# Kernel optimization log

Measured on AMD Instinct MI355X. Metric: run time of the kernel, lower is better.

## Reference

```python
import jax, jax.numpy as jnp
import numpy as np

B, N, D_IN, D_OUT = 32, 256, 512, 2048
RANK, K, H_CTRL = 12, 16, 192
RESIDUAL_SCALE = 1.0


def setup_inputs() -> dict:
    key = jax.random.key(0)
    ks = jax.random.split(key, 12)
    x = jax.random.normal(ks[0], (B, N, D_IN), dtype=jnp.float32)
    shared_weight = 0.02 * jax.random.normal(ks[1], (D_OUT, D_IN), dtype=jnp.float32)
    bias = jnp.zeros((D_OUT,), dtype=jnp.float32)
    # orthogonal init for U_0 [out, in] via QR of a Gaussian
    g = jax.random.normal(ks[2], (D_OUT, D_IN), dtype=jnp.float32)
    U0, _ = jnp.linalg.qr(g, mode='reduced')  # columns orthonormal, out>=in
    left_basis = 0.02 * jax.random.normal(ks[3], (K, D_OUT, RANK), dtype=jnp.float32)
    right_basis = 0.02 * jax.random.normal(ks[4], (K, D_IN, RANK), dtype=jnp.float32)
    ctrl_dim = 3 * D_IN  # cls_mean_var pooling
    W1 = (1.0 / np.sqrt(ctrl_dim)) * jax.random.normal(ks[5], (ctrl_dim, H_CTRL), dtype=jnp.float32)
    b1 = jnp.zeros((H_CTRL,), dtype=jnp.float32)
    Wc = (1.0 / np.sqrt(H_CTRL)) * jax.random.normal(ks[6], (H_CTRL, K), dtype=jnp.float32)
    bc = jnp.zeros((K,), dtype=jnp.float32)
    Wg = (1.0 / np.sqrt(H_CTRL)) * jax.random.normal(ks[7], (H_CTRL, 1), dtype=jnp.float32)
    bg = jnp.zeros((1,), dtype=jnp.float32)
    return {"x": x, "shared_weight": shared_weight, "bias": bias, "U0": U0,
            "left_basis": left_basis, "right_basis": right_basis,
            "W1": W1, "b1": b1, "Wc": Wc, "bc": bc, "Wg": Wg, "bg": bg}


def _controller(z, W1, b1, Wc, bc, Wg, bg):
    # MLP controller: coeff head (linear) + gate head (sigmoid)
    h = jax.nn.gelu(z @ W1 + b1)
    coeff = h @ Wc + bc            # [B, K]
    gate = jax.nn.sigmoid(h @ Wg + bg)  # [B, 1]
    return coeff, gate


def reference(x, shared_weight, bias, U0, left_basis, right_basis, W1, b1, Wc, bc, Wg, bg):
    # conditioning signal: cls + mean + var (unbiased=False)
    cls = x[:, 0]
    mean = x.mean(axis=1)
    var = x.var(axis=1)  # population variance, matches unbiased=False
    z = jnp.concatenate([cls, mean, var], axis=-1)  # [B, 3*D_IN]
    coeff, gate = _controller(z, W1, b1, Wc, bc, Wg, bg)

    # tangent dictionary
    raw = jnp.einsum('kmr,kdr->kmd', left_basis, right_basis)        # [K, M, D]
    ut_raw = jnp.einsum('mi,kmj->kij', U0, raw)                       # U0^T @ raw: [K, D, D]
    sym = 0.5 * (ut_raw + jnp.swapaxes(ut_raw, -2, -1))
    tangent = raw - jnp.einsum('mi,kij->kmj', U0, sym)                # [K, M, D]
    norm = jnp.sqrt(jnp.sum(tangent * tangent, axis=(1, 2), keepdims=True))
    tangent = tangent / jnp.maximum(norm, 1e-6)

    # per-sample candidate + QR retraction (Stiefel)
    delta = jnp.einsum('bk,kmd->bmd', coeff, tangent)                 # [B, M, D]
    candidate = U0[None] + RESIDUAL_SCALE * delta
    q, r = jnp.linalg.qr(candidate, mode='reduced')                   # q: [B, M, D]
    sign = jnp.sign(jnp.diagonal(r, axis1=-2, axis2=-1))              # [B, D]
    sign = jnp.where(sign == 0, jnp.ones_like(sign), sign)
    dynamic_weight = q * sign[..., None, :]
    residual_weight = dynamic_weight - U0[None]                       # [B, M, D]

    out = x @ shared_weight.T + bias                                  # [B, N, M]
    residual_out = jnp.einsum('bnd,bmd->bnm', x, residual_weight)     # [B, N, M]
    return out + gate.reshape(-1, 1, 1) * residual_out
```

## Files before the change

### kernel.cpp

```cpp
#include <hip/hip_runtime.h>
#include <math.h>

#define B_    32
#define N_    256
#define DIN   512
#define DOUT  2048
#define RANK_ 12
#define K_    16
#define HC    192
#define CD    1536
#define P1    192
#define P2    384

typedef short short8 __attribute__((ext_vector_type(8)));
typedef float f32x4 __attribute__((ext_vector_type(4)));

__device__ inline short bf16r(float f) {
  unsigned u = __float_as_uint(f);
  unsigned r = (u + 0x7FFFu + ((u >> 16) & 1u)) >> 16;
  return (short)r;
}
__device__ inline float b16f(short s) {
  unsigned u = ((unsigned)(unsigned short)s) << 16;
  return __uint_as_float(u);
}

__global__ void k_stats(const float* __restrict__ x, float* __restrict__ z) {
  int b = blockIdx.x, d = threadIdx.x;
  const float* xb = x + (size_t)b * N_ * DIN;
  float s = 0.f, s2 = 0.f;
  for (int n = 0; n < N_; ++n) {
    float t = xb[(size_t)n * DIN + d];
    s += t; s2 += t * t;
  }
  float mean = s * (1.0f / N_);
  float var = s2 * (1.0f / N_) - mean * mean;
  float* zb = z + (size_t)b * CD;
  zb[d] = xb[d];
  zb[DIN + d] = mean;
  zb[2 * DIN + d] = var;
}

__global__ void k_controller(const float* __restrict__ z, const float* __restrict__ W1,
                             const float* __restrict__ b1, const float* __restrict__ Wc,
                             const float* __restrict__ bc, const float* __restrict__ Wg,
                             const float* __restrict__ bg, float* __restrict__ coeff,
                             float* __restrict__ gate) {
  int b = blockIdx.x, j = threadIdx.x;
  __shared__ float zs[CD];
  __shared__ float hs[HC];
  const float* zb = z + (size_t)b * CD;
  for (int i = j; i < CD; i += HC) zs[i] = zb[i];
  __syncthreads();
  float acc = b1[j];
  for (int d = 0; d < CD; ++d) acc = fmaf(zs[d], W1[(size_t)d * HC + j], acc);
  float x3 = acc * acc * acc;
  float hj = 0.5f * acc * (1.0f + tanhf(0.7978845608028654f * (acc + 0.044715f * x3)));
  hs[j] = hj;
  __syncthreads();
  if (j < K_) {
    float c = bc[j];
    for (int t = 0; t < HC; ++t) c = fmaf(hs[t], Wc[t * K_ + j], c);
    coeff[b * K_ + j] = c;
  } else if (j == K_) {
    float g = bg[0];
    for (int t = 0; t < HC; ++t) g = fmaf(hs[t], Wg[t], g);
    gate[b] = 1.0f / (1.0f + expf(-g));
  }
}

__global__ void k_copy_bases(const float* __restrict__ leftb, const float* __restrict__ rightb,
                             float* __restrict__ Lcat, float* __restrict__ E) {
  int idx = blockIdx.x * 256 + threadIdx.x;
  const int totL = DOUT * P1;
  const int totR = DIN * P1;
  if (idx < totL) {
    int m = idx / P1, j = idx - m * P1;
    int k = j / RANK_, r = j - k * RANK_;
    Lcat[idx] = leftb[((size_t)k * DOUT + m) * RANK_ + r];
  } else if (idx < totL + totR) {
    int i2 = idx - totL;
    int d = i2 / P1, j = i2 - d * P1;
    int k = j / RANK_, r = j - k * RANK_;
    E[(size_t)d * P2 + j] = rightb[((size_t)k * DIN + d) * RANK_ + r];
  }
}

__global__ void k_pack_B(const float* __restrict__ Wsh, const float* __restrict__ U0,
                         const float* __restrict__ LcatF, short* __restrict__ Bcat) {
  int idx = blockIdx.x * 256 + threadIdx.x;
  if (idx >= DOUT * 152) return;
  int row = idx / 152, g = idx - row * 152;
  const float* src;
  if (g < 64)       src = Wsh + (size_t)row * DIN + g * 8;
  else if (g < 128) src = U0 + (size_t)row * DIN + (g - 64) * 8;
  else              src = LcatF + (size_t)row * P1 + (g - 128) * 8;
  short8 o;
#pragma unroll
  for (int e = 0; e < 8; ++e) o[e] = bf16r(src[e]);
  *(short8*)(Bcat + (size_t)row * 1216 + g * 8) = o;
}

__global__ __launch_bounds__(256) void k_gemm_tn(const float* __restrict__ A,
                                                 const float* __restrict__ B,
                                                 float* __restrict__ C,
                                                 int M, int N, int Kd, int lda, int ldb, int ldc) {
  __shared__ float As[32][33], Bs[32][33];
  int i0 = blockIdx.x * 32, j0 = blockIdx.y * 32;
  int t = threadIdx.x;
  int ii = t & 31, j4 = (t >> 5) * 4;
  float acc[4] = {0.f, 0.f, 0.f, 0.f};
  for (int kb = 0; kb < Kd; kb += 32) {
    for (int idx = t; idx < 1024; idx += 256) {
      int kk = idx >> 5, c = idx & 31;
      As[kk][c] = A[(size_t)(kb + kk) * lda + i0 + c];
      Bs[kk][c] = B[(size_t)(kb + kk) * ldb + j0 + c];
    }
    __syncthreads();
#pragma unroll 8
    for (int kk = 0; kk < 32; ++kk) {
      float a = As[kk][ii];
#pragma unroll
      for (int q = 0; q < 4; ++q) acc[q] = fmaf(a, Bs[kk][j4 + q], acc[q]);
    }
    __syncthreads();
  }
#pragma unroll
  for (int q = 0; q < 4; ++q) C[(size_t)(i0 + ii) * ldc + j0 + j4 + q] = acc[q];
}

__global__ void k_norms(const float* __restrict__ GLL, const float* __restrict__ GE,
                        float* __restrict__ norms) {
  int k = blockIdx.x, t = threadIdx.x;
  float s1 = 0.f, s2 = 0.f, s3 = 0.f;
  for (int idx = t; idx < RANK_ * RANK_; idx += 64) {
    int r = idx / RANK_, s = idx - r * RANK_;
    int p = k * RANK_ + r, q = k * RANK_ + s;
    float gll = GLL[p * P1 + q];
    float grr = GE[p * P2 + q];
    float gpp = GE[(P1 + p) * P2 + (P1 + q)];
    float gpr = GE[(P1 + p) * P2 + q];
    float gprt = GE[(P1 + q) * P2 + p];
    s1 += gll * grr;
    s2 += gpp * grr;
    s3 += gpr * gprt;
  }
#pragma unroll
  for (int off = 32; off > 0; off >>= 1) {
    s1 += __shfl_down(s1, off);
    s2 += __shfl_down(s2, off);
    s3 += __shfl_down(s3, off);
  }
  if (t == 0) norms[k] = sqrtf(fmaxf(s1 - 0.5f * (s2 + s3), 0.0f));
}

__global__ void k_cprime(const float* __restrict__ coeff, const float* __restrict__ norms,
                         float* __restrict__ cp) {
  int t = threadIdx.x;
  if (t < B_ * K_) {
    int k = t & 15;
    cp[t] = coeff[t] / fmaxf(norms[k], 1e-6f);
  }
}

__global__ void k_m0b(const float* __restrict__ GLL, const float* __restrict__ GE,
                      short* __restrict__ M0b) {
  int idx = blockIdx.x * 256 + threadIdx.x;
  if (idx >= P2 * P2) return;
  int p = idx / P2, q = idx - p * P2;
  float v;
  if (p < P1) {
    if (q < P1) v = GLL[p * P1 + q] - 0.75f * GE[(P1 + p) * P2 + (P1 + q)];
    else        v = -0.25f * GE[(P1 + p) * P2 + (q - P1)];
  } else {
    if (q < P1) v = -0.25f * GE[(P1 + q) * P2 + (p - P1)];
    else        v = 0.25f * GE[(p - P1) * P2 + (q - P1)];
  }
  M0b[idx] = bf16r(v);
}

__global__ void k_packE(const float* __restrict__ E, short* __restrict__ Eb16,
                        short* __restrict__ Etb16) {
  int idx = blockIdx.x * 256 + threadIdx.x;
  if (idx >= DIN * P2) return;
  int d = idx / P2, q = idx - d * P2;
  short v = bf16r(E[idx]);
  Eb16[idx] = v;
  Etb16[(size_t)q * DIN + d] = v;
}

__global__ void k_packEc(const float* __restrict__ E, const float* __restrict__ cp,
                         short* __restrict__ Ecb) {
  int idx = blockIdx.x * 256 + threadIdx.x;
  if (idx >= B_ * DIN * 48) return;
  int b = idx / (DIN * 48);
  int rem = idx - b * DIN * 48;
  int d = rem / 48, g = rem - d * 48;
  int q0 = g * 8;
  const float* src = E + (size_t)d * P2 + q0;
  const float* cpb = cp + b * K_;
  short8 o;
#pragma unroll
  for (int e = 0; e < 8; ++e) {
    int q = q0 + e;
    int kidx = (q % P1) / RANK_;
    o[e] = bf16r(src[e] * cpb[kidx]);
  }
  *(short8*)(Ecb + ((size_t)b * DIN + d) * P2 + q0) = o;
}

template<int MSZ, int NSZ, int KD>
__global__ __launch_bounds__(256) void k_mf_nt16(const short* __restrict__ A,
                                                 const short* __restrict__ B,
                                                 short* __restrict__ C) {
  int b = blockIdx.z;
  const short* Ab = A + (size_t)b * MSZ * KD;
  short* Cb = C + (size_t)b * MSZ * NSZ;
  int c0 = blockIdx.x * 64, r0 = blockIdx.y * 64;
  __shared__ short As[64][40], Bs[64][40];
  int t = threadIdx.x;
  int l = t & 63, wid = t >> 6;
  int wr = wid >> 1, wc = wid & 1;
  int fr = l & 15, fq = l >> 4;
  int row = t >> 2, cg = t & 3;
  f32x4 acc[2][2] = {};
  for (int kt = 0; kt < KD / 32; ++kt) {
    *(short8*)&As[row][cg * 8] = *(const short8*)(Ab + (size_t)(r0 + row) * KD + kt * 32 + cg * 8);
    *(short8*)&Bs[row][cg * 8] = *(const short8*)(B + (size_t)(c0 + row) * KD + kt * 32 + cg * 8);
    __syncthreads();
    short8 af[2], bf[2];
#pragma unroll
    for (int m = 0; m < 2; ++m) af[m] = *(const short8*)&As[wr * 32 + m * 16 + fr][fq * 8];
#pragma unroll
    for (int n = 0; n < 2; ++n) bf[n] = *(const short8*)&Bs[wc * 32 + n * 16 + fr][fq * 8];
#pragma unroll
    for (int m = 0; m < 2; ++m)
#pragma unroll
      for (int n = 0; n < 2; ++n)
        acc[m][n] = __builtin_amdgcn_mfma_f32_16x16x32_bf16(af[m], bf[n], acc[m][n], 0, 0, 0);
    __syncthreads();
  }
#pragma unroll
  for (int m = 0; m < 2; ++m)
#pragma unroll
    for (int n = 0; n < 2; ++n)
#pragma unroll
      for (int j = 0; j < 4; ++j)
        Cb[(size_t)(r0 + wr * 32 + m * 16 + fq * 4 + j) * NSZ + c0 + wc * 32 + n * 16 + fr] =
            bf16r(acc[m][n][j]);
}

__global__ __launch_bounds__(256) void k_mf_G(const short* __restrict__ H,
                                              const short* __restrict__ Ec,
                                              float* __restrict__ G) {
  int b = blockIdx.z;
  const short* Ab = H + (size_t)b * DIN * P2;
  const short* Bb = Ec + (size_t)b * DIN * P2;
  float* Gb = G + (size_t)b * DIN * DIN;
  int c0 = blockIdx.x * 64, r0 = blockIdx.y * 64;
  __shared__ short As[64][40], Bs[64][40];
  int t = threadIdx.x;
  int l = t & 63, wid = t >> 6;
  int wr = wid >> 1, wc = wid & 1;
  int fr = l & 15, fq = l >> 4;
  int row = t >> 2, cg = t & 3;
  f32x4 acc[2][2] = {};
  for (int kt = 0; kt < P2 / 32; ++kt) {
    *(short8*)&As[row][cg * 8] = *(const short8*)(Ab + (size_t)(r0 + row) * P2 + kt * 32 + cg * 8);
    *(short8*)&Bs[row][cg * 8] = *(const short8*)(Bb + (size_t)(c0 + row) * P2 + kt * 32 + cg * 8);
    __syncthreads();
    short8 af[2], bf[2];
#pragma unroll
    for (int m = 0; m < 2; ++m) af[m] = *(const short8*)&As[wr * 32 + m * 16 + fr][fq * 8];
#pragma unroll
    for (int n = 0; n < 2; ++n) bf[n] = *(const short8*)&Bs[wc * 32 + n * 16 + fr][fq * 8];
#pragma unroll
    for (int m = 0; m < 2; ++m)
#pragma unroll
      for (int n = 0; n < 2; ++n)
        acc[m][n] = __builtin_amdgcn_mfma_f32_16x16x32_bf16(af[m], bf[n], acc[m][n], 0, 0, 0);
    __syncthreads();
  }
#pragma unroll
  for (int m = 0; m < 2; ++m)
#pragma unroll
    for (int n = 0; n < 2; ++n)
#pragma unroll
      for (int j = 0; j < 4; ++j) {
        int gr = r0 + wr * 32 + m * 16 + fq * 4 + j;
        int gc = c0 + wc * 32 + n * 16 + fr;
        Gb[(size_t)gr * DIN + gc] = acc[m][n][j] + (gr == gc ? 1.0f : 0.0f);
      }
}

__global__ __launch_bounds__(64) void k_chol_dp2(float* __restrict__ G, float* __restrict__ Wd,
                                                 int j0) {
  int b = blockIdx.y;
  int role = blockIdx.x;
  float* Gb = G + (size_t)b * DIN * DIN;
  __shared__ float D[64][65];
  __shared__ float Wls[64][65];
  __shared__ float dinvs[64];
  int t = threadIdx.x;
#pragma unroll 8
  for (int i = 0; i < 64; ++i) D[i][t] = Gb[(size_t)(j0 + i) * DIN + j0 + t];
  __syncthreads();
  {
    float col[64];
#pragma unroll
    for (int i = 0; i < 64; ++i) col[i] = D[i][t];
#pragma unroll
    for (int j = 0; j < 64; ++j) {
      float djj = __shfl(col[j], j);
      float rjj = sqrtf(fmaxf(djj, 1e-30f));
      float rinv = 1.0f / rjj;
      if (t == j) col[j] = rjj;
      else if (t > j) col[j] *= rinv;
      float djt = col[j];
#pragma unroll
      for (int i = j + 1; i < 64; ++i) {
        float rji = __shfl(col[j], i);
        if (i <= t) col[i] = fmaf(-rji, djt, col[i]);
      }
    }
#pragma unroll
    for (int i = 0; i < 64; ++i) D[i][t] = (i <= t) ? col[i] : 0.0f;
    dinvs[t] = 1.0f / col[t];
  }
  __syncthreads();
  if (role == 0) {
#pragma unroll 4
    for (int i = 0; i < 64; ++i) Wls[i][t] = 0.0f;
    Wls[t][t] = dinvs[t];
    for (int i = 62; i >= 0; --i) {
      float s = 0.0f;
      for (int j = i + 1; j < 64; ++j) s = fmaf(D[i][j], Wls[j][t], s);
      if (t > i) Wls[i][t] = -s * dinvs[i];
    }
    float* Wp = Wd + ((size_t)b * 8 + (j0 >> 6)) * 4096;
#pragma unroll 4
    for (int i = 0; i < 64; ++i) Wp[i * 64 + t] = Wls[i][t];
  } else {
    int c = j0 + 64 + (role - 1) * 64 + t;
    float a[64];
#pragma unroll
    for (int i = 0; i < 64; ++i) a[i] = Gb[(size_t)(j0 + i) * DIN + c];
#pragma unroll
    for (int j = 0; j < 64; ++j) {
      float aj = a[j] * dinvs[j];
      a[j] = aj;
#pragma unroll
      for (int i = j + 1; i < 64; ++i) a[i] = fmaf(-D[j][i], aj, a[i]);
    }
#pragma unroll
    for (int i = 0; i < 64; ++i) Gb[(size_t)(j0 + i) * DIN + c] = a[i];
  }
}

__global__ __launch_bounds__(256) void k_chol_tr(float* __restrict__ G, int j0, int nt) {
  int b = blockIdx.y;
  int pi = blockIdx.x;
  int ti = 0, accum = 0;
  while (pi >= accum + (nt - ti)) { accum += nt - ti; ++ti; }
  int tc = ti + (pi - accum);
  float* Gb = G + (size_t)b * DIN * DIN;
  __shared__ float As[64][65], Bs[64][65];
  int t = threadIdx.x;
  int ibase = j0 + 64 + ti * 64, cbase = j0 + 64 + tc * 64;
  for (int idx = t; idx < 4096; idx += 256) {
    int j = idx >> 6, c = idx & 63;
    As[j][c] = Gb[(size_t)(j0 + j) * DIN + ibase + c];
    Bs[j][c] = Gb[(size_t)(j0 + j) * DIN + cbase + c];
  }
  __syncthreads();
  int tx = t & 15, ty = t >> 4;
  float acc[4][4] = {};
#pragma unroll 8
  for (int k = 0; k < 64; ++k) {
    float a[4], bv[4];
#pragma unroll
    for (int u = 0; u < 4; ++u) a[u] = As[k][ty * 4 + u];
#pragma unroll
    for (int v = 0; v < 4; ++v) bv[v] = Bs[k][tx * 4 + v];
#pragma unroll
    for (int u = 0; u < 4; ++u)
#pragma unroll
      for (int v = 0; v < 4; ++v) acc[u][v] = fmaf(a[u], bv[v], acc[u][v]);
  }
#pragma unroll
  for (int u = 0; u < 4; ++u) {
    size_t ro = (size_t)(ibase + ty * 4 + u) * DIN + cbase + tx * 4;
#pragma unroll
    for (int v = 0; v < 4; ++v) Gb[ro + v] -= acc[u][v];
  }
}

__global__ __launch_bounds__(256) void k_trif(const float* __restrict__ x, const float* __restrict__ G,
                                              const float* __restrict__ Wd, short* __restrict__ ybf,
                                              short* __restrict__ ycb) {
  int b = blockIdx.y;
  int n0 = blockIdx.x * 16;
  const float* R = G + (size_t)b * DIN * DIN;
  const float* xb = x + ((size_t)b * N_ + n0) * DIN;
  __shared__ float Yl[16][517];
  __shared__ float Rs[16][65];
  __shared__ float Wds[64][65];
  __shared__ float Ytmp[16][69];
  int t = threadIdx.x;
  for (int idx = t; idx < 16 * DIN; idx += 256)
    Yl[idx >> 9][idx & 511] = xb[(size_t)(idx >> 9) * DIN + (idx & 511)];
  __syncthreads();
  int r = t & 15, cg = t >> 4;
  for (int p = 7; p >= 0; --p) {
    int j0 = p * 64;
    int kN = DIN - j0 - 64;
    float acc[4] = {0.f, 0.f, 0.f, 0.f};
    for (int kb = 0; kb < kN; kb += 16) {
      for (int idx = t; idx < 1024; idx += 256) {
        int kk = idx & 15, c = idx >> 4;
        Rs[kk][c] = R[(size_t)(j0 + c) * DIN + j0 + 64 + kb + kk];
      }
      __syncthreads();
#pragma unroll
      for (int kk = 0; kk < 16; ++kk) {
        float a = Yl[r][j0 + 64 + kb + kk];
#pragma unroll
        for (int v = 0; v < 4; ++v) acc[v] = fmaf(a, Rs[kk][cg * 4 + v], acc[v]);
      }
      __syncthreads();
    }
#pragma unroll
    for (int v = 0; v < 4; ++v) Ytmp[r][cg * 4 + v] = Yl[r][j0 + cg * 4 + v] - acc[v];
    const float* Wp = Wd + ((size_t)b * 8 + p) * 4096;
    for (int idx = t; idx < 4096; idx += 256) Wds[idx >> 6][idx & 63] = Wp[idx];
    __syncthreads();
    float o[4] = {0.f, 0.f, 0.f, 0.f};
#pragma unroll 8
    for (int jj = 0; jj < 64; ++jj) {
      float a = Ytmp[r][jj];
#pragma unroll
      for (int v = 0; v < 4; ++v) o[v] = fmaf(a, Wds[cg * 4 + v][jj], o[v]);
    }
    __syncthreads();
#pragma unroll
    for (int v = 0; v < 4; ++v) Yl[r][j0 + cg * 4 + v] = o[v];
    __syncthreads();
  }
  for (int idx = t; idx < 16 * DIN; idx += 256) {
    int rr = idx >> 9, c = idx & 511;
    float yv = Yl[rr][c];
    float xv = xb[(size_t)rr * DIN + c];
    size_t gi = ((size_t)b * N_ + n0 + rr) * DIN + c;
    ybf[gi] = bf16r(yv);
    ycb[gi] = bf16r(yv - xv);
  }
}

__global__ void k_uv2(const float* __restrict__ cp, const float* __restrict__ gate,
                      const short* __restrict__ yE16, short* __restrict__ vb) {
  int idx = blockIdx.x * 256 + threadIdx.x;
  if (idx >= B_ * N_ * P1) return;
  int q = idx % P1;
  int bn = idx / P1;
  int b = bn >> 8;
  float yR = b16f(yE16[(size_t)bn * P2 + q]);
  vb[idx] = bf16r(gate[b] * cp[b * K_ + q / RANK_] * yR);
}

__global__ __launch_bounds__(256) void k_mf_w(const short* __restrict__ yE16,
                                              const short* __restrict__ Eb,
                                              const short* __restrict__ ycb,
                                              const float* __restrict__ cp,
                                              const float* __restrict__ gate,
                                              short* __restrict__ wb) {
  int b = blockIdx.z;
  const short* yEb = yE16 + (size_t)b * N_ * P2;
  int c0 = blockIdx.x * 64, r0 = blockIdx.y * 64;
  __shared__ short As[64][40], Bs[64][40];
  __shared__ float cps[K_];
  int t = threadIdx.x;
  if (t < K_) cps[t] = 0.5f * cp[b * K_ + t];
  int l = t & 63, wid = t >> 6;
  int wr = wid >> 1, wc = wid & 1;
  int fr = l & 15, fq = l >> 4;
  int row = t >> 2, cg = t & 3;
  f32x4 acc[2][2] = {};
  __syncthreads();
  for (int kt = 0; kt < P2 / 32; ++kt) {
    int ksrc0 = (kt * 32 + P1) % P2;
    short8 raw = *(const short8*)(yEb + (size_t)(r0 + row) * P2 + ksrc0 + cg * 8);
    short8 oa;
#pragma unroll
    for (int e = 0; e < 8; ++e) {
      int q = kt * 32 + cg * 8 + e;
      int kidx = (q % P1) / RANK_;
      oa[e] = bf16r(b16f(raw[e]) * cps[kidx]);
    }
    *(short8*)&As[row][cg * 8] = oa;
    *(short8*)&Bs[row][cg * 8] = *(const short8*)(Eb + (size_t)(c0 + row) * P2 + kt * 32 + cg * 8);
    __syncthreads();
    short8 af[2], bf[2];
#pragma unroll
    for (int m = 0; m < 2; ++m) af[m] = *(const short8*)&As[wr * 32 + m * 16 + fr][fq * 8];
#pragma unroll
    for (int n = 0; n < 2; ++n) bf[n] = *(const short8*)&Bs[wc * 32 + n * 16 + fr][fq * 8];
#pragma unroll
    for (int m = 0; m < 2; ++m)
#pragma unroll
      for (int n = 0; n < 2; ++n)
        acc[m][n] = __builtin_amdgcn_mfma_f32_16x16x32_bf16(af[m], bf[n], acc[m][n], 0, 0, 0);
    __syncthreads();
  }
  float gt = gate[b];
#pragma unroll
  for (int m = 0; m < 2; ++m)
#pragma unroll
    for (int n = 0; n < 2; ++n)
#pragma unroll
      for (int j = 0; j < 4; ++j) {
        int gr = r0 + wr * 32 + m * 16 + fq * 4 + j;
        int gc = c0 + wc * 32 + n * 16 + fr;
        size_t gi = ((size_t)b * N_ + gr) * DIN + gc;
        wb[gi] = bf16r(gt * (b16f(ycb[gi]) - acc[m][n][j]));
      }
}

__device__ inline short8 loadA8(const float* __restrict__ x, const short* __restrict__ wb,
                                const short* __restrict__ vb, int grow, int k0) {
  if (k0 < 512) {
    const float* p = x + (size_t)grow * 512 + k0;
    float4 f0 = *(const float4*)p;
    float4 f1 = *(const float4*)(p + 4);
    short8 o;
    o[0] = bf16r(f0.x); o[1] = bf16r(f0.y); o[2] = bf16r(f0.z); o[3] = bf16r(f0.w);
    o[4] = bf16r(f1.x); o[5] = bf16r(f1.y); o[6] = bf16r(f1.z); o[7] = bf16r(f1.w);
    return o;
  } else if (k0 < 1024) {
    return *(const short8*)(wb + (size_t)grow * 512 + k0 - 512);
  } else {
    return *(const short8*)(vb + (size_t)grow * 192 + k0 - 1024);
  }
}

__global__ __launch_bounds__(256) void k_final(
    const float* __restrict__ x, const short* __restrict__ wb, const short* __restrict__ vb,
    const short* __restrict__ Bcat, const float* __restrict__ bias, float* __restrict__ out) {
  __shared__ short As[2][4096];
  __shared__ short Bs[2][4096];
  int t = threadIdx.x;
  int c0 = blockIdx.x * 128;
  int r0 = blockIdx.y * 128;
  int l = t & 63, wid = t >> 6;
  int wr = wid >> 1, wc = wid & 1;
  int fr = l & 15, fq = l >> 4;
  f32x4 acc[4][4] = {};
  short8 ra0, ra1, rb0, rb1;
  const int row0 = t >> 2, c8 = t & 3;
  const int row1 = row0 + 64;
  ra0 = loadA8(x, wb, vb, r0 + row0, c8 * 8);
  ra1 = loadA8(x, wb, vb, r0 + row1, c8 * 8);
  rb0 = *(const short8*)(Bcat + (size_t)(c0 + row0) * 1216 + c8 * 8);
  rb1 = *(const short8*)(Bcat + (size_t)(c0 + row1) * 1216 + c8 * 8);
  *(short8*)&As[0][row0 * 32 + c8 * 8] = ra0;
  *(short8*)&As[0][row1 * 32 + c8 * 8] = ra1;
  *(short8*)&Bs[0][row0 * 32 + c8 * 8] = rb0;
  *(short8*)&Bs[0][row1 * 32 + c8 * 8] = rb1;
  __syncthreads();
  for (int kt = 0; kt < 38; ++kt) {
    int cur = kt & 1;
    if (kt + 1 < 38) {
      int k0 = (kt + 1) * 32;
      ra0 = loadA8(x, wb, vb, r0 + row0, k0 + c8 * 8);
      ra1 = loadA8(x, wb, vb, r0 + row1, k0 + c8 * 8);
      rb0 = *(const short8*)(Bcat + (size_t)(c0 + row0) * 1216 + k0 + c8 * 8);
      rb1 = *(const short8*)(Bcat + (size_t)(c0 + row1) * 1216 + k0 + c8 * 8);
    }
    short8 af[4], bf[4];
#pragma unroll
    for (int m = 0; m < 4; ++m)
      af[m] = *(const short8*)&As[cur][(wr * 64 + m * 16 + fr) * 32 + fq * 8];
#pragma unroll
    for (int n = 0; n < 4; ++n)
      bf[n] = *(const short8*)&Bs[cur][(wc * 64 + n * 16 + fr) * 32 + fq * 8];
#pragma unroll
    for (int m = 0; m < 4; ++m)
#pragma unroll
      for (int n = 0; n < 4; ++n)
        acc[m][n] = __builtin_amdgcn_mfma_f32_16x16x32_bf16(af[m], bf[n], acc[m][n], 0, 0, 0);
    __syncthreads();
    if (kt + 1 < 38) {
      int nxt = cur ^ 1;
      *(short8*)&As[nxt][row0 * 32 + c8 * 8] = ra0;
      *(short8*)&As[nxt][row1 * 32 + c8 * 8] = ra1;
      *(short8*)&Bs[nxt][row0 * 32 + c8 * 8] = rb0;
      *(short8*)&Bs[nxt][row1 * 32 + c8 * 8] = rb1;
    }
    __syncthreads();
  }
#pragma unroll
  for (int n = 0; n < 4; ++n) {
    int col = c0 + wc * 64 + n * 16 + fr;
    float bv = bias[col];
#pragma unroll
    for (int m = 0; m < 4; ++m) {
      int rbase = r0 + wr * 64 + m * 16 + fq * 4;
#pragma unroll
      for (int j = 0; j < 4; ++j)
        out[(size_t)(rbase + j) * DOUT + col] = acc[m][n][j] + bv;
    }
  }
}

extern "C" void kernel_launch(void* const* d_in, const int* in_sizes, int n_in,
                              void* d_out, int out_size, void* d_ws, size_t ws_size,
                              hipStream_t stream) {
  (void)in_sizes; (void)n_in; (void)out_size; (void)ws_size;
  const float* x     = (const float*)d_in[0];
  const float* Wsh   = (const float*)d_in[1];
  const float* bias  = (const float*)d_in[2];
  const float* U0    = (const float*)d_in[3];
  const float* leftb = (const float*)d_in[4];
  const float* rightb= (const float*)d_in[5];
  const float* W1    = (const float*)d_in[6];
  const float* b1    = (const float*)d_in[7];
  const float* Wc    = (const float*)d_in[8];
  const float* bc    = (const float*)d_in[9];
  const float* Wg    = (const float*)d_in[10];
  const float* bg    = (const float*)d_in[11];
  float* out = (float*)d_out;

  float* wsf = (float*)d_ws;
  float* z     = wsf + 0;
  float* coeff = wsf + 49152;
  float* gate  = wsf + 49664;
  float* norms = wsf + 49728;
  float* cp    = wsf + 49792;
  float* LcatF = wsf + 50304;
  float* E     = wsf + 443520;
  float* GLL   = wsf + 640128;
  float* GE    = wsf + 676992;
  short* M0b16 = (short*)(wsf + 824448);
  short* Eb16  = (short*)(wsf + 898176);
  short* Etb16 = (short*)(wsf + 996480);
  short* wb    = (short*)(wsf + 1094784);
  short* Ecb   = (short*)(wsf + 3191936);
  short* ybf   = (short*)(wsf + 3191936);
  short* vb    = (short*)(wsf + 5289088);
  short* Hb16  = (short*)(wsf + 6337664);
  short* ycb   = (short*)(wsf + 6337664);
  short* Bcat  = (short*)(wsf + 9483392);
  float* G = out;
  float* Wd = out + 8388608;
  short* yE16 = (short*)(out + 8388608 + 1048576);

  k_stats<<<B_, DIN, 0, stream>>>(x, z);
  k_controller<<<B_, HC, 0, stream>>>(z, W1, b1, Wc, bc, Wg, bg, coeff, gate);
  k_copy_bases<<<(DOUT * P1 + DIN * P1 + 255) / 256, 256, 0, stream>>>(leftb, rightb, LcatF, E);
  k_pack_B<<<(DOUT * 152 + 255) / 256, 256, 0, stream>>>(Wsh, U0, LcatF, Bcat);
  k_gemm_tn<<<dim3(DIN / 32, P1 / 32), 256, 0, stream>>>(U0, LcatF, E + P1, DIN, P1, DOUT, DIN, P1, P2);
  k_gemm_tn<<<dim3(P1 / 32, P1 / 32), 256, 0, stream>>>(LcatF, LcatF, GLL, P1, P1, DOUT, P1, P1, P1);
  k_gemm_tn<<<dim3(P2 / 32, P2 / 32), 256, 0, stream>>>(E, E, GE, P2, P2, DIN, P2, P2, P2);
  k_norms<<<K_, 64, 0, stream>>>(GLL, GE, norms);
  k_cprime<<<1, 512, 0, stream>>>(coeff, norms, cp);
  k_m0b<<<(P2 * P2 + 255) / 256, 256, 0, stream>>>(GLL, GE, M0b16);
  k_packE<<<(DIN * P2 + 255) / 256, 256, 0, stream>>>(E, Eb16, Etb16);
  k_packEc<<<(B_ * DIN * 48 + 255) / 256, 256, 0, stream>>>(E, cp, Ecb);
  k_mf_nt16<DIN, P2, P2><<<dim3(P2 / 64, DIN / 64, B_), 256, 0, stream>>>(Ecb, M0b16, Hb16);
  k_mf_G<<<dim3(DIN / 64, DIN / 64, B_), 256, 0, stream>>>(Hb16, Ecb, G);
  for (int p = 0; p < 8; ++p) {
    int j0 = p * 64;
    int nt = 7 - p;
    k_chol_dp2<<<dim3(nt + 1, B_), 64, 0, stream>>>(G, Wd, j0);
    if (nt > 0)
      k_chol_tr<<<dim3(nt * (nt + 1) / 2, B_), 256, 0, stream>>>(G, j0, nt);
  }
  k_trif<<<dim3(N_ / 16, B_), 256, 0, stream>>>(x, G, Wd, ybf, ycb);
  k_mf_nt16<N_, P2, DIN><<<dim3(P2 / 64, N_ / 64, B_), 256, 0, stream>>>(ybf, Etb16, yE16);
  k_uv2<<<(B_ * N_ * P1 + 255) / 256, 256, 0, stream>>>(cp, gate, yE16, vb);
  k_mf_w<<<dim3(DIN / 64, N_ / 64, B_), 256, 0, stream>>>(yE16, Eb16, ycb, cp, gate, wb);
  k_final<<<dim3(DOUT / 128, (B_ * N_) / 128), 256, 0, stream>>>(x, wb, vb, Bcat, bias, out);
}
```

Baseline: 1.745 ms.

## Merge preprocessing kernels into fewer launches and fuse yE GEMM with uv epilogue

Folds the twelve small preprocessing launches (stats, controller, base copies, packing, small GEMMs, norms, cprime, M0/Ec packing) into five multi-role kernels that dispatch work by block index. Independent stages now share a launch. It also fuses the yE bf16 GEMM with the gate/coefficient scaling that produces vb, which removes one pass over yE. Separately, the triangular-solve kernel now stages 64-wide R tiles instead of 16-wide ones, so it synchronises less often but uses more shared memory per block.

```diff
diff --git a/kernel.cpp b/kernel.cpp
--- a/kernel.cpp
+++ b/kernel.cpp
@@ -25,89 +25,50 @@
   return __uint_as_float(u);
 }
 
-__global__ void k_stats(const float* __restrict__ x, float* __restrict__ z) {
-  int b = blockIdx.x, d = threadIdx.x;
-  const float* xb = x + (size_t)b * N_ * DIN;
-  float s = 0.f, s2 = 0.f;
-  for (int n = 0; n < N_; ++n) {
-    float t = xb[(size_t)n * DIN + d];
-    s += t; s2 += t * t;
-  }
-  float mean = s * (1.0f / N_);
-  float var = s2 * (1.0f / N_) - mean * mean;
-  float* zb = z + (size_t)b * CD;
-  zb[d] = xb[d];
-  zb[DIN + d] = mean;
-  zb[2 * DIN + d] = var;
-}
-
-__global__ void k_controller(const float* __restrict__ z, const float* __restrict__ W1,
-                             const float* __restrict__ b1, const float* __restrict__ Wc,
-                             const float* __restrict__ bc, const float* __restrict__ Wg,
-                             const float* __restrict__ bg, float* __restrict__ coeff,
-                             float* __restrict__ gate) {
-  int b = blockIdx.x, j = threadIdx.x;
-  __shared__ float zs[CD];
-  __shared__ float hs[HC];
-  const float* zb = z + (size_t)b * CD;
-  for (int i = j; i < CD; i += HC) zs[i] = zb[i];
-  __syncthreads();
-  float acc = b1[j];
-  for (int d = 0; d < CD; ++d) acc = fmaf(zs[d], W1[(size_t)d * HC + j], acc);
-  float x3 = acc * acc * acc;
-  float hj = 0.5f * acc * (1.0f + tanhf(0.7978845608028654f * (acc + 0.044715f * x3)));
-  hs[j] = hj;
-  __syncthreads();
-  if (j < K_) {
-    float c = bc[j];
-    for (int t = 0; t < HC; ++t) c = fmaf(hs[t], Wc[t * K_ + j], c);
-    coeff[b * K_ + j] = c;
-  } else if (j == K_) {
-    float g = bg[0];
-    for (int t = 0; t < HC; ++t) g = fmaf(hs[t], Wg[t], g);
-    gate[b] = 1.0f / (1.0f + expf(-g));
-  }
-}
-
-__global__ void k_copy_bases(const float* __restrict__ leftb, const float* __restrict__ rightb,
-                             float* __restrict__ Lcat, float* __restrict__ E) {
-  int idx = blockIdx.x * 256 + threadIdx.x;
-  const int totL = DOUT * P1;
-  const int totR = DIN * P1;
-  if (idx < totL) {
-    int m = idx / P1, j = idx - m * P1;
-    int k = j / RANK_, r = j - k * RANK_;
-    Lcat[idx] = leftb[((size_t)k * DOUT + m) * RANK_ + r];
-  } else if (idx < totL + totR) {
-    int i2 = idx - totL;
-    int d = i2 / P1, j = i2 - d * P1;
-    int k = j / RANK_, r = j - k * RANK_;
-    E[(size_t)d * P2 + j] = rightb[((size_t)k * DIN + d) * RANK_ + r];
-  }
-}
-
-__global__ void k_pack_B(const float* __restrict__ Wsh, const float* __restrict__ U0,
-                         const float* __restrict__ LcatF, short* __restrict__ Bcat) {
-  int idx = blockIdx.x * 256 + threadIdx.x;
-  if (idx >= DOUT * 152) return;
-  int row = idx / 152, g = idx - row * 152;
-  const float* src;
-  if (g < 64)       src = Wsh + (size_t)row * DIN + g * 8;
-  else if (g < 128) src = U0 + (size_t)row * DIN + (g - 64) * 8;
-  else              src = LcatF + (size_t)row * P1 + (g - 128) * 8;
-  short8 o;
-#pragma unroll
-  for (int e = 0; e < 8; ++e) o[e] = bf16r(src[e]);
-  *(short8*)(Bcat + (size_t)row * 1216 + g * 8) = o;
-}
-
-__global__ __launch_bounds__(256) void k_gemm_tn(const float* __restrict__ A,
-                                                 const float* __restrict__ B,
-                                                 float* __restrict__ C,
-                                                 int M, int N, int Kd, int lda, int ldb, int ldc) {
-  __shared__ float As[32][33], Bs[32][33];
-  int i0 = blockIdx.x * 32, j0 = blockIdx.y * 32;
-  int t = threadIdx.x;
+__global__ __launch_bounds__(256) void k_pre1(const float* __restrict__ x,
+                                              const float* __restrict__ leftb,
+                                              const float* __restrict__ rightb,
+                                              float* __restrict__ z, float* __restrict__ Lcat,
+                                              float* __restrict__ E) {
+  int bx = blockIdx.x, t = threadIdx.x;
+  if (bx < B_) {
+    const float* xb = x + (size_t)bx * N_ * DIN;
+    float* zb = z + (size_t)bx * CD;
+#pragma unroll
+    for (int h = 0; h < 2; ++h) {
+      int d = t + h * 256;
+      float s = 0.f, s2 = 0.f;
+      for (int n = 0; n < N_; ++n) {
+        float v = xb[(size_t)n * DIN + d];
+        s += v; s2 += v * v;
+      }
+      float mean = s * (1.0f / N_);
+      float var = s2 * (1.0f / N_) - mean * mean;
+      zb[d] = xb[d];
+      zb[DIN + d] = mean;
+      zb[2 * DIN + d] = var;
+    }
+  } else {
+    int idx = (bx - B_) * 256 + t;
+    const int totL = DOUT * P1;
+    const int totR = DIN * P1;
+    if (idx < totL) {
+      int m = idx / P1, j = idx - m * P1;
+      int k = j / RANK_, r = j - k * RANK_;
+      Lcat[idx] = leftb[((size_t)k * DOUT + m) * RANK_ + r];
+    } else if (idx < totL + totR) {
+      int i2 = idx - totL;
+      int d = i2 / P1, j = i2 - d * P1;
+      int k = j / RANK_, r = j - k * RANK_;
+      E[(size_t)d * P2 + j] = rightb[((size_t)k * DIN + d) * RANK_ + r];
+    }
+  }
+}
+
+__device__ inline void gemm_tn_body(const float* __restrict__ A, const float* __restrict__ B,
+                                    float* __restrict__ C, int i0, int j0, int Kd,
+                                    int lda, int ldb, int ldc,
+                                    float (*As)[33], float (*Bs)[33], int t) {
   int ii = t & 31, j4 = (t >> 5) * 4;
   float acc[4] = {0.f, 0.f, 0.f, 0.f};
   for (int kb = 0; kb < Kd; kb += 32) {
@@ -129,11 +90,82 @@
   for (int q = 0; q < 4; ++q) C[(size_t)(i0 + ii) * ldc + j0 + j4 + q] = acc[q];
 }
 
-__global__ void k_norms(const float* __restrict__ GLL, const float* __restrict__ GE,
-                        float* __restrict__ norms) {
-  int k = blockIdx.x, t = threadIdx.x;
+__global__ __launch_bounds__(256) void k_pre2(const float* __restrict__ z,
+                                              const float* __restrict__ W1, const float* __restrict__ b1,
+                                              const float* __restrict__ Wc, const float* __restrict__ bc,
+                                              const float* __restrict__ Wg, const float* __restrict__ bg,
+                                              const float* __restrict__ U0, const float* __restrict__ LcatF,
+                                              float* __restrict__ coeff, float* __restrict__ gate,
+                                              float* __restrict__ E, float* __restrict__ GLL) {
+  int bx = blockIdx.x, t = threadIdx.x;
+  __shared__ float As[32][33], Bs[32][33];
+  __shared__ float zs[CD];
+  __shared__ float hs[HC];
+  if (bx < B_) {
+    const float* zb = z + (size_t)bx * CD;
+    for (int i = t; i < CD; i += 256) zs[i] = zb[i];
+    __syncthreads();
+    if (t < HC) {
+      float acc = b1[t];
+      for (int d = 0; d < CD; ++d) acc = fmaf(zs[d], W1[(size_t)d * HC + t], acc);
+      float x3 = acc * acc * acc;
+      hs[t] = 0.5f * acc * (1.0f + tanhf(0.7978845608028654f * (acc + 0.044715f * x3)));
+    }
+    __syncthreads();
+    if (t < K_) {
+      float c = bc[t];
+      for (int q = 0; q < HC; ++q) c = fmaf(hs[q], Wc[q * K_ + t], c);
+      coeff[bx * K_ + t] = c;
+    } else if (t == K_) {
+      float g = bg[0];
+      for (int q = 0; q < HC; ++q) g = fmaf(hs[q], Wg[q], g);
+      gate[bx] = 1.0f / (1.0f + expf(-g));
+    }
+  } else if (bx < 128) {
+    int idx = bx - 32;
+    gemm_tn_body(U0, LcatF, E + P1, (idx & 15) * 32, (idx >> 4) * 32, DOUT, DIN, P1, P2, As, Bs, t);
+  } else {
+    int idx = bx - 128;
+    gemm_tn_body(LcatF, LcatF, GLL, (idx % 6) * 32, (idx / 6) * 32, DOUT, P1, P1, P1, As, Bs, t);
+  }
+}
+
+__global__ __launch_bounds__(256) void k_pre3(const float* __restrict__ E,
+                                              const float* __restrict__ Wsh, const float* __restrict__ U0,
+                                              const float* __restrict__ LcatF,
+                                              float* __restrict__ GE, short* __restrict__ Bcat,
+                                              short* __restrict__ Eb16, short* __restrict__ Etb16) {
+  int bx = blockIdx.x, t = threadIdx.x;
+  __shared__ float As[32][33], Bs[32][33];
+  if (bx < 144) {
+    gemm_tn_body(E, E, GE, (bx % 12) * 32, (bx / 12) * 32, DIN, P2, P2, P2, As, Bs, t);
+  } else if (bx < 1360) {
+    int idx = (bx - 144) * 256 + t;
+    int row = idx / 152, g = idx - row * 152;
+    const float* src;
+    if (g < 64)       src = Wsh + (size_t)row * DIN + g * 8;
+    else if (g < 128) src = U0 + (size_t)row * DIN + (g - 64) * 8;
+    else              src = LcatF + (size_t)row * P1 + (g - 128) * 8;
+    short8 o;
+#pragma unroll
+    for (int e = 0; e < 8; ++e) o[e] = bf16r(src[e]);
+    *(short8*)(Bcat + (size_t)row * 1216 + g * 8) = o;
+  } else {
+    int idx = (bx - 1360) * 256 + t;
+    int d = idx / P2, q = idx - d * P2;
+    short v = bf16r(E[idx]);
+    Eb16[idx] = v;
+    Etb16[(size_t)q * DIN + d] = v;
+  }
+}
+
+__global__ __launch_bounds__(512) void k_pre4(const float* __restrict__ GLL, const float* __restrict__ GE,
+                                              const float* __restrict__ coeff,
+                                              float* __restrict__ norms, float* __restrict__ cp) {
+  int t = threadIdx.x;
+  int k = t >> 5, lane = t & 31;
   float s1 = 0.f, s2 = 0.f, s3 = 0.f;
-  for (int idx = t; idx < RANK_ * RANK_; idx += 64) {
+  for (int idx = lane; idx < RANK_ * RANK_; idx += 32) {
     int r = idx / RANK_, s = idx - r * RANK_;
     int p = k * RANK_ + r, q = k * RANK_ + s;
     float gll = GLL[p * P1 + q];
@@ -146,67 +178,50 @@
     s3 += gpr * gprt;
   }
 #pragma unroll
-  for (int off = 32; off > 0; off >>= 1) {
-    s1 += __shfl_down(s1, off);
-    s2 += __shfl_down(s2, off);
-    s3 += __shfl_down(s3, off);
-  }
-  if (t == 0) norms[k] = sqrtf(fmaxf(s1 - 0.5f * (s2 + s3), 0.0f));
-}
-
-__global__ void k_cprime(const float* __restrict__ coeff, const float* __restrict__ norms,
-                         float* __restrict__ cp) {
-  int t = threadIdx.x;
-  if (t < B_ * K_) {
-    int k = t & 15;
-    cp[t] = coeff[t] / fmaxf(norms[k], 1e-6f);
-  }
-}
-
-__global__ void k_m0b(const float* __restrict__ GLL, const float* __restrict__ GE,
-                      short* __restrict__ M0b) {
-  int idx = blockIdx.x * 256 + threadIdx.x;
-  if (idx >= P2 * P2) return;
-  int p = idx / P2, q = idx - p * P2;
-  float v;
-  if (p < P1) {
-    if (q < P1) v = GLL[p * P1 + q] - 0.75f * GE[(P1 + p) * P2 + (P1 + q)];
-    else        v = -0.25f * GE[(P1 + p) * P2 + (q - P1)];
+  for (int off = 16; off > 0; off >>= 1) {
+    s1 += __shfl_down(s1, off, 32);
+    s2 += __shfl_down(s2, off, 32);
+    s3 += __shfl_down(s3, off, 32);
+  }
+  if (lane == 0) norms[k] = sqrtf(fmaxf(s1 - 0.5f * (s2 + s3), 0.0f));
+  __syncthreads();
+  cp[t] = coeff[t] / fmaxf(norms[t & 15], 1e-6f);
+}
+
+__global__ __launch_bounds__(256) void k_pre5(const float* __restrict__ GLL, const float* __restrict__ GE,
+                                              const float* __restrict__ E, const float* __restrict__ cp,
+                                              short* __restrict__ M0b, short* __restrict__ Ecb) {
+  int bx = blockIdx.x, t = threadIdx.x;
+  if (bx < 576) {
+    int idx = bx * 256 + t;
+    if (idx >= P2 * P2) return;
+    int p = idx / P2, q = idx - p * P2;
+    float v;
+    if (p < P1) {
+      if (q < P1) v = GLL[p * P1 + q] - 0.75f * GE[(P1 + p) * P2 + (P1 + q)];
+      else        v = -0.25f * GE[(P1 + p) * P2 + (q - P1)];
+    } else {
+      if (q < P1) v = -0.25f * GE[(P1 + q) * P2 + (p - P1)];
+      else        v = 0.25f * GE[(p - P1) * P2 + (q - P1)];
+    }
+    M0b[idx] = bf16r(v);
   } else {
-    if (q < P1) v = -0.25f * GE[(P1 + q) * P2 + (p - P1)];
-    else        v = 0.25f * GE[(p - P1) * P2 + (q - P1)];
-  }
-  M0b[idx] = bf16r(v);
-}
-
-__global__ void k_packE(const float* __restrict__ E, short* __restrict__ Eb16,
-                        short* __restrict__ Etb16) {
-  int idx = blockIdx.x * 256 + threadIdx.x;
-  if (idx >= DIN * P2) return;
-  int d = idx / P2, q = idx - d * P2;
-  short v = bf16r(E[idx]);
-  Eb16[idx] = v;
-  Etb16[(size_t)q * DIN + d] = v;
-}
-
-__global__ void k_packEc(const float* __restrict__ E, const float* __restrict__ cp,
-                         short* __restrict__ Ecb) {
-  int idx = blockIdx.x * 256 + threadIdx.x;
-  if (idx >= B_ * DIN * 48) return;
-  int b = idx / (DIN * 48);
-  int rem = idx - b * DIN * 48;
-  int d = rem / 48, g = rem - d * 48;
-  int q0 = g * 8;
-  const float* src = E + (size_t)d * P2 + q0;
-  const float* cpb = cp + b * K_;
-  short8 o;
-#pragma unroll
-  for (int e = 0; e < 8; ++e) {
-    int q = q0 + e;
-    int kidx = (q % P1) / RANK_;
-    o[e] = bf16r(src[e] * cpb[kidx]);
-  }
-  *(short8*)(Ecb + ((size_t)b * DIN + d) * P2 + q0) = o;
+    int idx = (bx - 576) * 256 + t;
+    int b = idx / (DIN * 48);
+    int rem = idx - b * DIN * 48;
+    int d = rem / 48, g = rem - d * 48;
+    int q0 = g * 8;
+    const float* src = E + (size_t)d * P2 + q0;
+    const float* cpb = cp + b * K_;
+    short8 o;
+#pragma unroll
+    for (int e = 0; e < 8; ++e) {
+      int q = q0 + e;
+      int kidx = (q % P1) / RANK_;
+      o[e] = bf16r(src[e] * cpb[kidx]);
+    }
+    *(short8*)(Ecb + ((size_t)b * DIN + d) * P2 + q0) = o;
+  }
 }
 
 template<int MSZ, int NSZ, int KD>
@@ -403,7 +418,7 @@
   const float* R = G + (size_t)b * DIN * DIN;
   const float* xb = x + ((size_t)b * N_ + n0) * DIN;
   __shared__ float Yl[16][517];
-  __shared__ float Rs[16][65];
+  __shared__ float Rs[64][65];
   __shared__ float Wds[64][65];
   __shared__ float Ytmp[16][69];
   int t = threadIdx.x;
@@ -415,14 +430,14 @@
     int j0 = p * 64;
     int kN = DIN - j0 - 64;
     float acc[4] = {0.f, 0.f, 0.f, 0.f};
-    for (int kb = 0; kb < kN; kb += 16) {
-      for (int idx = t; idx < 1024; idx += 256) {
-        int kk = idx & 15, c = idx >> 4;
+    for (int kb = 0; kb < kN; kb += 64) {
+      for (int idx = t; idx < 4096; idx += 256) {
+        int kk = idx & 63, c = idx >> 6;
         Rs[kk][c] = R[(size_t)(j0 + c) * DIN + j0 + 64 + kb + kk];
       }
       __syncthreads();
-#pragma unroll
-      for (int kk = 0; kk < 16; ++kk) {
+#pragma unroll 8
+      for (int kk = 0; kk < 64; ++kk) {
         float a = Yl[r][j0 + 64 + kb + kk];
 #pragma unroll
         for (int v = 0; v < 4; ++v) acc[v] = fmaf(a, Rs[kk][cg * 4 + v], acc[v]);
@@ -456,15 +471,55 @@
   }
 }
 
-__global__ void k_uv2(const float* __restrict__ cp, const float* __restrict__ gate,
-                      const short* __restrict__ yE16, short* __restrict__ vb) {
-  int idx = blockIdx.x * 256 + threadIdx.x;
-  if (idx >= B_ * N_ * P1) return;
-  int q = idx % P1;
-  int bn = idx / P1;
-  int b = bn >> 8;
-  float yR = b16f(yE16[(size_t)bn * P2 + q]);
-  vb[idx] = bf16r(gate[b] * cp[b * K_ + q / RANK_] * yR);
+__global__ __launch_bounds__(256) void k_yEuv(const short* __restrict__ A,
+                                              const short* __restrict__ B,
+                                              const float* __restrict__ cp,
+                                              const float* __restrict__ gate,
+                                              short* __restrict__ C, short* __restrict__ vb) {
+  int b = blockIdx.z;
+  const short* Ab = A + (size_t)b * N_ * DIN;
+  short* Cb = C + (size_t)b * N_ * P2;
+  int c0 = blockIdx.x * 64, r0 = blockIdx.y * 64;
+  __shared__ short As[64][40], Bs[64][40];
+  __shared__ float cps[K_];
+  int t = threadIdx.x;
+  if (t < K_) cps[t] = cp[b * K_ + t];
+  int l = t & 63, wid = t >> 6;
+  int wr = wid >> 1, wc = wid & 1;
+  int fr = l & 15, fq = l >> 4;
+  int row = t >> 2, cg = t & 3;
+  f32x4 acc[2][2] = {};
+  __syncthreads();
+  for (int kt = 0; kt < DIN / 32; ++kt) {
+    *(short8*)&As[row][cg * 8] = *(const short8*)(Ab + (size_t)(r0 + row) * DIN + kt * 32 + cg * 8);
+    *(short8*)&Bs[row][cg * 8] = *(const short8*)(B + (size_t)(c0 + row) * DIN + kt * 32 + cg * 8);
+    __syncthreads();
+    short8 af[2], bf[2];
+#pragma unroll
+    for (int m = 0; m < 2; ++m) af[m] = *(const short8*)&As[wr * 32 + m * 16 + fr][fq * 8];
+#pragma unroll
+    for (int n = 0; n < 2; ++n) bf[n] = *(const short8*)&Bs[wc * 32 + n * 16 + fr][fq * 8];
+#pragma unroll
+    for (int m = 0; m < 2; ++m)
+#pragma unroll
+      for (int n = 0; n < 2; ++n)
+        acc[m][n] = __builtin_amdgcn_mfma_f32_16x16x32_bf16(af[m], bf[n], acc[m][n], 0, 0, 0);
+    __syncthreads();
+  }
+  float gt = gate[b];
+#pragma unroll
+  for (int m = 0; m < 2; ++m)
+#pragma unroll
+    for (int n = 0; n < 2; ++n)
+#pragma unroll
+      for (int j = 0; j < 4; ++j) {
+        int gr = r0 + wr * 32 + m * 16 + fq * 4 + j;
+        int gc = c0 + wc * 32 + n * 16 + fr;
+        float v = acc[m][n][j];
+        Cb[(size_t)gr * P2 + gc] = bf16r(v);
+        if (gc < P1)
+          vb[((size_t)b * N_ + gr) * P1 + gc] = bf16r(gt * cps[gc / RANK_] * v);
+      }
 }
 
 __global__ __launch_bounds__(256) void k_mf_w(const short* __restrict__ yE16,
@@ -653,18 +708,11 @@
   float* Wd = out + 8388608;
   short* yE16 = (short*)(out + 8388608 + 1048576);
 
-  k_stats<<<B_, DIN, 0, stream>>>(x, z);
-  k_controller<<<B_, HC, 0, stream>>>(z, W1, b1, Wc, bc, Wg, bg, coeff, gate);
-  k_copy_bases<<<(DOUT * P1 + DIN * P1 + 255) / 256, 256, 0, stream>>>(leftb, rightb, LcatF, E);
-  k_pack_B<<<(DOUT * 152 + 255) / 256, 256, 0, stream>>>(Wsh, U0, LcatF, Bcat);
-  k_gemm_tn<<<dim3(DIN / 32, P1 / 32), 256, 0, stream>>>(U0, LcatF, E + P1, DIN, P1, DOUT, DIN, P1, P2);
-  k_gemm_tn<<<dim3(P1 / 32, P1 / 32), 256, 0, stream>>>(LcatF, LcatF, GLL, P1, P1, DOUT, P1, P1, P1);
-  k_gemm_tn<<<dim3(P2 / 32, P2 / 32), 256, 0, stream>>>(E, E, GE, P2, P2, DIN, P2, P2, P2);
-  k_norms<<<K_, 64, 0, stream>>>(GLL, GE, norms);
-  k_cprime<<<1, 512, 0, stream>>>(coeff, norms, cp);
-  k_m0b<<<(P2 * P2 + 255) / 256, 256, 0, stream>>>(GLL, GE, M0b16);
-  k_packE<<<(DIN * P2 + 255) / 256, 256, 0, stream>>>(E, Eb16, Etb16);
-  k_packEc<<<(B_ * DIN * 48 + 255) / 256, 256, 0, stream>>>(E, cp, Ecb);
+  k_pre1<<<32 + 1920, 256, 0, stream>>>(x, leftb, rightb, z, LcatF, E);
+  k_pre2<<<164, 256, 0, stream>>>(z, W1, b1, Wc, bc, Wg, bg, U0, LcatF, coeff, gate, E, GLL);
+  k_pre3<<<2128, 256, 0, stream>>>(E, Wsh, U0, LcatF, GE, Bcat, Eb16, Etb16);
+  k_pre4<<<1, 512, 0, stream>>>(GLL, GE, coeff, norms, cp);
+  k_pre5<<<3648, 256, 0, stream>>>(GLL, GE, E, cp, M0b16, Ecb);
   k_mf_nt16<DIN, P2, P2><<<dim3(P2 / 64, DIN / 64, B_), 256, 0, stream>>>(Ecb, M0b16, Hb16);
   k_mf_G<<<dim3(DIN / 64, DIN / 64, B_), 256, 0, stream>>>(Hb16, Ecb, G);
   for (int p = 0; p < 8; ++p) {
@@ -675,8 +723,7 @@
       k_chol_tr<<<dim3(nt * (nt + 1) / 2, B_), 256, 0, stream>>>(G, j0, nt);
   }
   k_trif<<<dim3(N_ / 16, B_), 256, 0, stream>>>(x, G, Wd, ybf, ycb);
-  k_mf_nt16<N_, P2, DIN><<<dim3(P2 / 64, N_ / 64, B_), 256, 0, stream>>>(ybf, Etb16, yE16);
-  k_uv2<<<(B_ * N_ * P1 + 255) / 256, 256, 0, stream>>>(cp, gate, yE16, vb);
+  k_yEuv<<<dim3(P2 / 64, N_ / 64, B_), 256, 0, stream>>>(ybf, Etb16, cp, gate, yE16, vb);
   k_mf_w<<<dim3(DIN / 64, N_ / 64, B_), 256, 0, stream>>>(yE16, Eb16, ycb, cp, gate, wb);
   k_final<<<dim3(DOUT / 128, (B_ * N_) / 128), 256, 0, stream>>>(x, wb, vb, Bcat, bias, out);
 }
```

After: 1.562 ms. 1.12x faster.
